# Optimization experiments

Measured on AMD Instinct MI355X. Metric: run time of the kernel, lower is better.

## Reference

```python
import jax, jax.numpy as jnp
import numpy as np

B, M, D, S, TOPK = 8, 4096, 512, 128, 64


def setup_inputs() -> dict:
    key = jax.random.key(0)
    ks = jax.random.split(key, 9)
    return {
        "memory": jax.random.normal(ks[0], (B, M, D), jnp.float32),
        "usage": jax.random.uniform(ks[1], (B, M), dtype=jnp.float32),
        "content": jax.random.normal(ks[2], (B, D), jnp.float32),
        "write_strength": jax.random.uniform(ks[3], (B, 1), dtype=jnp.float32),
        "query": jax.random.normal(ks[4], (B, S, D), jnp.float32),
        "key_proj_w": jax.random.normal(ks[5], (D, D), jnp.float32) * 0.02,
        "temporal_table": jax.random.normal(ks[6], (M, D), jnp.float32) * 0.02,
        "usage_decay": jnp.float32(0.99),
        "valid_mask": jax.random.randint(ks[7], (B, M), 0, 2) > 0,
        "write_index": jax.random.randint(ks[8], (B,), 0, M),
        "top_k": TOPK,
    }


def reference(memory, usage, content, write_strength, query, key_proj_w,
              temporal_table, usage_decay, valid_mask, write_index, top_k):
    # ---- write(): soft scatter into the slot selected by write_index ----
    idx = write_index % M                               # [B]
    temporal_emb = temporal_table[idx]                  # [B, D] gather
    content_wt = content + temporal_emb                 # [B, D]
    write_pos = jax.nn.one_hot(idx, M, dtype=memory.dtype)      # [B, M]
    a = write_pos[:, :, None] * write_strength[:, :, None]      # [B, M, 1]
    memory = memory * (1.0 - a) + content_wt[:, None, :] * a    # [B, M, D]
    valid = jnp.logical_or(valid_mask, write_pos > 0)           # [B, M]
    usage = usage * usage_decay + write_pos * write_strength    # [B, M]
    # ---- read(): content-based addressing with top-k masked softmax ----
    keys = jnp.einsum("bmd,ed->bme", memory, key_proj_w)        # Linear, no bias
    scores = jnp.einsum("bsd,bmd->bsm", query, keys) / (D ** 0.5)
    scores = jnp.where(valid[:, None, :], scores, -jnp.inf)
    top_vals = jax.lax.top_k(scores, top_k)[0]                  # [B, S, top_k]
    threshold = top_vals[..., -1:]                              # kth value
    scores = jnp.where(scores < threshold, -jnp.inf, scores)
    attn = jax.nn.softmax(scores, axis=-1)                      # [B, S, M]
    all_invalid = jnp.all(~valid, axis=-1)[:, None, None]
    attn = jnp.where(all_invalid, 0.0, attn)
    retrieved = jnp.einsum("bsm,bmd->bsd", attn, memory)        # [B, S, D]
    return retrieved, attn, usage
```

## Files before the change

kernel.cpp:

```cpp
#include <hip/hip_runtime.h>
#include <hip/hip_bf16.h>
#include <math.h>

#define BB 8
#define MM 4096
#define DD 512
#define SS 128

typedef short s16x8 __attribute__((ext_vector_type(8)));
typedef float f32x4 __attribute__((ext_vector_type(4)));

__device__ __forceinline__ unsigned short f2bf(float x) {
  unsigned u = __float_as_uint(x);
  unsigned r = u + 0x7fffu + ((u >> 16) & 1u);
  return (unsigned short)(r >> 16);
}
__device__ __forceinline__ float bf2f(unsigned short h) {
  return __uint_as_float(((unsigned)h) << 16);
}
__device__ __forceinline__ void split3(float x, unsigned short& s1,
                                       unsigned short& s2, unsigned short& s3) {
  s1 = f2bf(x);
  float r1 = x - bf2f(s1);
  s2 = f2bf(r1);
  float r2 = r1 - bf2f(s2);
  s3 = f2bf(r2);
}

__global__ __launch_bounds__(256) void update_kernel(
    float* __restrict__ memory, const float* __restrict__ usage,
    const float* __restrict__ content, const float* __restrict__ wstr,
    const float* __restrict__ ttab, const float* __restrict__ decay_p,
    const int* __restrict__ widx, float* __restrict__ usage_out) {
  const int b = blockIdx.x;
  int idx = widx[b] % MM; if (idx < 0) idx += MM;
  const float ws = wstr[b];
  const float decay = decay_p[0];
  for (int d = threadIdx.x; d < DD; d += blockDim.x) {
    float cw = content[b * DD + d] + ttab[(size_t)idx * DD + d];
    size_t off = (size_t)b * MM * DD + (size_t)idx * DD + d;
    float old = memory[off];
    memory[off] = old * (1.0f - ws) + cw * ws;
  }
  for (int m = threadIdx.x; m < MM; m += blockDim.x) {
    float u = usage[b * MM + m] * decay;
    if (m == idx) u += ws;
    usage_out[b * MM + m] = u;
  }
}

#define BMq 64
#define BNq 64
#define BKq 32
#define PADq 4

__global__ __launch_bounds__(256) void gemm_nn_qp(
    const float* __restrict__ A, const float* __restrict__ Bw,
    unsigned short* __restrict__ q1, unsigned short* __restrict__ q2,
    unsigned short* __restrict__ q3) {
  __shared__ __align__(16) float As[BKq][BMq + PADq];
  __shared__ __align__(16) float Bs[BKq][BNq + PADq];
  const int tid = threadIdx.x;
  const int tx = tid & 15, ty = tid >> 4;
  const int i0 = blockIdx.y * BMq;
  const int j0 = blockIdx.x * BNq;
  float acc[4][4] = {{0.f}};
  for (int k0 = 0; k0 < DD; k0 += BKq) {
#pragma unroll
    for (int r = 0; r < 2; ++r) {
      int ff = tid + r * 256;
      int row = ff >> 3, kq = ff & 7;
      float4 v = *(const float4*)(A + (size_t)(i0 + row) * DD + k0 + kq * 4);
      As[kq * 4 + 0][row] = v.x; As[kq * 4 + 1][row] = v.y;
      As[kq * 4 + 2][row] = v.z; As[kq * 4 + 3][row] = v.w;
      int kr = ff >> 4, jq = ff & 15;
      float4 w = *(const float4*)(Bw + (size_t)(k0 + kr) * DD + j0 + jq * 4);
      *(float4*)&Bs[kr][jq * 4] = w;
    }
    __syncthreads();
#pragma unroll
    for (int k = 0; k < BKq; ++k) {
      float4 a = *(const float4*)&As[k][ty * 4];
      float4 bb = *(const float4*)&Bs[k][tx * 4];
      float av[4] = {a.x, a.y, a.z, a.w};
      float bv[4] = {bb.x, bb.y, bb.z, bb.w};
#pragma unroll
      for (int i = 0; i < 4; ++i)
#pragma unroll
        for (int j = 0; j < 4; ++j) acc[i][j] += av[i] * bv[j];
    }
    __syncthreads();
  }
#pragma unroll
  for (int i = 0; i < 4; ++i) {
    int row = i0 + ty * 4 + i;
    ushort4 v1, v2, v3;
    split3(acc[i][0], v1.x, v2.x, v3.x);
    split3(acc[i][1], v1.y, v2.y, v3.y);
    split3(acc[i][2], v1.z, v2.z, v3.z);
    split3(acc[i][3], v1.w, v2.w, v3.w);
    *(ushort4*)(q1 + (size_t)row * DD + j0 + tx * 4) = v1;
    *(ushort4*)(q2 + (size_t)row * DD + j0 + tx * 4) = v2;
    *(ushort4*)(q3 + (size_t)row * DD + j0 + tx * 4) = v3;
  }
}

#define LSTR 40

__global__ __launch_bounds__(256, 2) void gemm_scores_mfma(
    const unsigned short* __restrict__ q1_g,
    const unsigned short* __restrict__ q2_g,
    const unsigned short* __restrict__ q3_g,
    const float* __restrict__ mem, float* __restrict__ sc_out) {
  __shared__ __align__(16) unsigned short q1_s[128 * LSTR];
  __shared__ __align__(16) unsigned short q2_s[128 * LSTR];
  __shared__ __align__(16) unsigned short q3_s[128 * LSTR];
  __shared__ __align__(16) unsigned short m1_s[64 * LSTR];
  __shared__ __align__(16) unsigned short m2_s[64 * LSTR];
  __shared__ __align__(16) unsigned short m3_s[64 * LSTR];
  const int tid = threadIdx.x;
  const int b = blockIdx.x & 7;
  const int j0 = (blockIdx.x >> 3) * 64;
  const int wv = tid >> 6, lane = tid & 63;
  const int quad = lane >> 4, r = lane & 15;

  const int qrow0 = tid >> 2, qc0 = tid & 3;
  const int qrow1 = (tid + 256) >> 2, qc1 = tid & 3;
  const unsigned short* q1b = q1_g + (size_t)b * SS * DD;
  const unsigned short* q2b = q2_g + (size_t)b * SS * DD;
  const unsigned short* q3b = q3_g + (size_t)b * SS * DD;
  const int mrow0 = tid >> 3, mk0 = tid & 7;
  const int mrow1 = (tid + 256) >> 3, mk1 = tid & 7;
  const float* mbase = mem + ((size_t)b * MM + j0) * DD;

  f32x4 accA[2][4], accB[2][4];
#pragma unroll
  for (int i = 0; i < 2; ++i)
#pragma unroll
    for (int j = 0; j < 4; ++j)
#pragma unroll
      for (int c = 0; c < 4; ++c) { accA[i][j][c] = 0.f; accB[i][j][c] = 0.f; }

  uint4 q1_r0, q1_r1, q2_r0, q2_r1, q3_r0, q3_r1;
  float4 m_r0, m_r1;

  q1_r0 = *(const uint4*)(q1b + (size_t)qrow0 * DD + qc0 * 8);
  q1_r1 = *(const uint4*)(q1b + (size_t)qrow1 * DD + qc1 * 8);
  q2_r0 = *(const uint4*)(q2b + (size_t)qrow0 * DD + qc0 * 8);
  q2_r1 = *(const uint4*)(q2b + (size_t)qrow1 * DD + qc1 * 8);
  q3_r0 = *(const uint4*)(q3b + (size_t)qrow0 * DD + qc0 * 8);
  q3_r1 = *(const uint4*)(q3b + (size_t)qrow1 * DD + qc1 * 8);
  m_r0 = *(const float4*)(mbase + (size_t)mrow0 * DD + mk0 * 4);
  m_r1 = *(const float4*)(mbase + (size_t)mrow1 * DD + mk1 * 4);

  for (int ks = 0; ks < 16; ++ks) {
    if (ks) __syncthreads();
    *(uint4*)&q1_s[qrow0 * LSTR + qc0 * 8] = q1_r0;
    *(uint4*)&q1_s[qrow1 * LSTR + qc1 * 8] = q1_r1;
    *(uint4*)&q2_s[qrow0 * LSTR + qc0 * 8] = q2_r0;
    *(uint4*)&q2_s[qrow1 * LSTR + qc1 * 8] = q2_r1;
    *(uint4*)&q3_s[qrow0 * LSTR + qc0 * 8] = q3_r0;
    *(uint4*)&q3_s[qrow1 * LSTR + qc1 * 8] = q3_r1;
    {
      ushort4 v1, v2, v3;
      split3(m_r0.x, v1.x, v2.x, v3.x);
      split3(m_r0.y, v1.y, v2.y, v3.y);
      split3(m_r0.z, v1.z, v2.z, v3.z);
      split3(m_r0.w, v1.w, v2.w, v3.w);
      *(ushort4*)&m1_s[mrow0 * LSTR + mk0 * 4] = v1;
      *(ushort4*)&m2_s[mrow0 * LSTR + mk0 * 4] = v2;
      *(ushort4*)&m3_s[mrow0 * LSTR + mk0 * 4] = v3;
      split3(m_r1.x, v1.x, v2.x, v3.x);
      split3(m_r1.y, v1.y, v2.y, v3.y);
      split3(m_r1.z, v1.z, v2.z, v3.z);
      split3(m_r1.w, v1.w, v2.w, v3.w);
      *(ushort4*)&m1_s[mrow1 * LSTR + mk1 * 4] = v1;
      *(ushort4*)&m2_s[mrow1 * LSTR + mk1 * 4] = v2;
      *(ushort4*)&m3_s[mrow1 * LSTR + mk1 * 4] = v3;
    }
    __syncthreads();
    if (ks < 15) {
      int k0 = (ks + 1) * 32;
      q1_r0 = *(const uint4*)(q1b + (size_t)qrow0 * DD + k0 + qc0 * 8);
      q1_r1 = *(const uint4*)(q1b + (size_t)qrow1 * DD + k0 + qc1 * 8);
      q2_r0 = *(const uint4*)(q2b + (size_t)qrow0 * DD + k0 + qc0 * 8);
      q2_r1 = *(const uint4*)(q2b + (size_t)qrow1 * DD + k0 + qc1 * 8);
      q3_r0 = *(const uint4*)(q3b + (size_t)qrow0 * DD + k0 + qc0 * 8);
      q3_r1 = *(const uint4*)(q3b + (size_t)qrow1 * DD + k0 + qc1 * 8);
      m_r0 = *(const float4*)(mbase + (size_t)mrow0 * DD + k0 + mk0 * 4);
      m_r1 = *(const float4*)(mbase + (size_t)mrow1 * DD + k0 + mk1 * 4);
    }
    s16x8 a1[2], a2[2], a3[2];
#pragma unroll
    for (int st = 0; st < 2; ++st) {
      int arow = wv * 32 + st * 16 + r;
      a1[st] = *(const s16x8*)&q1_s[arow * LSTR + quad * 8];
      a2[st] = *(const s16x8*)&q2_s[arow * LSTR + quad * 8];
      a3[st] = *(const s16x8*)&q3_s[arow * LSTR + quad * 8];
    }
#pragma unroll
    for (int jt = 0; jt < 4; ++jt) {
      int brow = jt * 16 + r;
      s16x8 b1 = *(const s16x8*)&m1_s[brow * LSTR + quad * 8];
      s16x8 b2 = *(const s16x8*)&m2_s[brow * LSTR + quad * 8];
      s16x8 b3 = *(const s16x8*)&m3_s[brow * LSTR + quad * 8];
#pragma unroll
      for (int st = 0; st < 2; ++st) {
        accB[st][jt] = __builtin_amdgcn_mfma_f32_16x16x32_bf16(a1[st], b3, accB[st][jt], 0, 0, 0);
        accB[st][jt] = __builtin_amdgcn_mfma_f32_16x16x32_bf16(a3[st], b1, accB[st][jt], 0, 0, 0);
        accB[st][jt] = __builtin_amdgcn_mfma_f32_16x16x32_bf16(a2[st], b2, accB[st][jt], 0, 0, 0);
        accB[st][jt] = __builtin_amdgcn_mfma_f32_16x16x32_bf16(a1[st], b2, accB[st][jt], 0, 0, 0);
        accB[st][jt] = __builtin_amdgcn_mfma_f32_16x16x32_bf16(a2[st], b1, accB[st][jt], 0, 0, 0);
        accA[st][jt] = __builtin_amdgcn_mfma_f32_16x16x32_bf16(a1[st], b1, accA[st][jt], 0, 0, 0);
      }
    }
  }
  const float scl = 0.04419417382415922f;
  float* C = sc_out + (size_t)b * SS * MM;
#pragma unroll
  for (int st = 0; st < 2; ++st)
#pragma unroll
    for (int jt = 0; jt < 4; ++jt)
#pragma unroll
      for (int reg = 0; reg < 4; ++reg) {
        int srow = wv * 32 + st * 16 + quad * 4 + reg;
        int scol = j0 + jt * 16 + r;
        C[(size_t)srow * MM + scol] = (accA[st][jt][reg] + accB[st][jt][reg]) * scl;
      }
}

__device__ __forceinline__ unsigned fkey(float f) {
  unsigned u = __float_as_uint(f);
  return (u & 0x80000000u) ? ~u : (u | 0x80000000u);
}
__device__ __forceinline__ float finv(unsigned u) {
  unsigned b = (u & 0x80000000u) ? (u & 0x7fffffffu) : ~u;
  return __uint_as_float(b);
}

__global__ __launch_bounds__(256) void select_kernel(
    const float* __restrict__ scores, const int* __restrict__ vmask,
    const int* __restrict__ widx, const int* __restrict__ topk,
    const float* __restrict__ memory, float* __restrict__ retrieved,
    float* __restrict__ attn) {
  __shared__ float sc[MM];
  __shared__ int kept[MM];
  __shared__ unsigned histw[4 * 256];
  __shared__ float red[256];
  __shared__ unsigned sh_pref;
  __shared__ int sh_k, sh_nkept;
  __shared__ float sh_zinv;

  const int tid = threadIdx.x;
  const int s = blockIdx.x, b = blockIdx.y;
  int wi = widx[b] % MM; if (wi < 0) wi += MM;
  const float4* srow4 = (const float4*)(scores + ((size_t)b * SS + s) * MM);
  const int4* vrow4 = (const int4*)(vmask + (size_t)b * MM);
  unsigned* hw = histw + (tid >> 6) * 256;

  if (tid == 0) { sh_pref = 0u; sh_nkept = 0; sh_k = topk[0]; }
  for (int i = tid; i < 1024; i += 256) histw[i] = 0u;
  __syncthreads();

  float lmax = -INFINITY;
  for (int m4 = tid; m4 < MM / 4; m4 += 256) {
    float4 v = srow4[m4];
    int4 mk = vrow4[m4];
    int mb = m4 * 4;
    if (!(mk.x || mb + 0 == wi)) v.x = -INFINITY;
    if (!(mk.y || mb + 1 == wi)) v.y = -INFINITY;
    if (!(mk.z || mb + 2 == wi)) v.z = -INFINITY;
    if (!(mk.w || mb + 3 == wi)) v.w = -INFINITY;
    ((float4*)sc)[m4] = v;
    lmax = fmaxf(lmax, fmaxf(fmaxf(v.x, v.y), fmaxf(v.z, v.w)));
    atomicAdd(&hw[fkey(v.x) >> 24], 1u);
    atomicAdd(&hw[fkey(v.y) >> 24], 1u);
    atomicAdd(&hw[fkey(v.z) >> 24], 1u);
    atomicAdd(&hw[fkey(v.w) >> 24], 1u);
  }
  red[tid] = lmax;
  __syncthreads();
#pragma unroll
  for (int off = 128; off > 0; off >>= 1) {
    if (tid < off) red[tid] = fmaxf(red[tid], red[tid + off]);
    __syncthreads();
  }
  const float maxv = red[0];

  for (int pass = 0; pass < 4; ++pass) {
    const int shift = 24 - pass * 8;
    if (pass > 0) {
      const unsigned pref = sh_pref;
      const unsigned hmask = 0xFFFFFFFFu << (shift + 8);
      for (int i = tid; i < 1024; i += 256) histw[i] = 0u;
      __syncthreads();
      for (int m = tid; m < MM; m += 256) {
        unsigned u = fkey(sc[m]);
        if ((u & hmask) == pref) atomicAdd(&hw[(u >> shift) & 0xFFu], 1u);
      }
      __syncthreads();
    }
    if (tid < 64) {
      const int l = tid;
      unsigned h0 = histw[l * 4 + 0] + histw[256 + l * 4 + 0] + histw[512 + l * 4 + 0] + histw[768 + l * 4 + 0];
      unsigned h1 = histw[l * 4 + 1] + histw[256 + l * 4 + 1] + histw[512 + l * 4 + 1] + histw[768 + l * 4 + 1];
      unsigned h2 = histw[l * 4 + 2] + histw[256 + l * 4 + 2] + histw[512 + l * 4 + 2] + histw[768 + l * 4 + 2];
      unsigned h3 = histw[l * 4 + 3] + histw[256 + l * 4 + 3] + histw[512 + l * 4 + 3] + histw[768 + l * 4 + 3];
      unsigned lsum = h0 + h1 + h2 + h3;
      unsigned g = lsum;
#pragma unroll
      for (int off = 1; off < 64; off <<= 1) {
        unsigned t = __shfl_down(g, off, 64);
        if (l + off < 64) g += t;
      }
      unsigned above = g - lsum;
      unsigned suf3 = h3 + above;
      unsigned suf2 = h2 + suf3;
      unsigned suf1 = h1 + suf2;
      unsigned suf0 = h0 + suf1;
      const unsigned kk = (unsigned)sh_k;
      const unsigned prefc = sh_pref;
      unsigned ge, geN;
      ge = suf0; geN = suf1;
      if (ge >= kk && geN < kk) { sh_pref = prefc | ((unsigned)(4 * l + 0) << shift); sh_k = (int)(kk - geN); }
      ge = suf1; geN = suf2;
      if (ge >= kk && geN < kk) { sh_pref = prefc | ((unsigned)(4 * l + 1) << shift); sh_k = (int)(kk - geN); }
      ge = suf2; geN = suf3;
      if (ge >= kk && geN < kk) { sh_pref = prefc | ((unsigned)(4 * l + 2) << shift); sh_k = (int)(kk - geN); }
      ge = suf3; geN = above;
      if (ge >= kk && geN < kk) { sh_pref = prefc | ((unsigned)(4 * l + 3) << shift); sh_k = (int)(kk - geN); }
    }
    __syncthreads();
  }
  const float thr = finv(sh_pref);

  float lz = 0.f;
  for (int m4 = tid; m4 < MM / 4; m4 += 256) {
    float4 v = ((float4*)sc)[m4];
    v.x = (v.x >= thr) ? __expf(v.x - maxv) : 0.f;
    v.y = (v.y >= thr) ? __expf(v.y - maxv) : 0.f;
    v.z = (v.z >= thr) ? __expf(v.z - maxv) : 0.f;
    v.w = (v.w >= thr) ? __expf(v.w - maxv) : 0.f;
    ((float4*)sc)[m4] = v;
    lz += v.x + v.y + v.z + v.w;
  }
  red[tid] = lz;
  __syncthreads();
#pragma unroll
  for (int off = 128; off > 0; off >>= 1) {
    if (tid < off) red[tid] += red[tid + off];
    __syncthreads();
  }
  if (tid == 0) sh_zinv = 1.0f / red[0];
  __syncthreads();
  const float zinv = sh_zinv;

  float4* arow4 = (float4*)(attn + ((size_t)b * SS + s) * MM);
  for (int m4 = tid; m4 < MM / 4; m4 += 256) {
    float4 p = ((float4*)sc)[m4];
    float4 o = make_float4(p.x * zinv, p.y * zinv, p.z * zinv, p.w * zinv);
    arow4[m4] = o;
    int mb = m4 * 4;
    if (p.x > 0.f) kept[atomicAdd(&sh_nkept, 1)] = mb + 0;
    if (p.y > 0.f) kept[atomicAdd(&sh_nkept, 1)] = mb + 1;
    if (p.z > 0.f) kept[atomicAdd(&sh_nkept, 1)] = mb + 2;
    if (p.w > 0.f) kept[atomicAdd(&sh_nkept, 1)] = mb + 3;
  }
  __syncthreads();
  const int nk = sh_nkept;

  float a0 = 0.f, a1 = 0.f;
  const float* mb_ = memory + (size_t)b * MM * DD;
  int i = 0;
  for (; i + 4 <= nk; i += 4) {
    int m0 = kept[i], m1 = kept[i + 1], m2 = kept[i + 2], m3 = kept[i + 3];
    float p0 = sc[m0], p1 = sc[m1], p2 = sc[m2], p3 = sc[m3];
    const float* r0 = mb_ + (size_t)m0 * DD;
    const float* r1 = mb_ + (size_t)m1 * DD;
    const float* r2 = mb_ + (size_t)m2 * DD;
    const float* r3 = mb_ + (size_t)m3 * DD;
    float v0a = r0[tid], v0b = r0[tid + 256];
    float v1a = r1[tid], v1b = r1[tid + 256];
    float v2a = r2[tid], v2b = r2[tid + 256];
    float v3a = r3[tid], v3b = r3[tid + 256];
    a0 += p0 * v0a + p1 * v1a + p2 * v2a + p3 * v3a;
    a1 += p0 * v0b + p1 * v1b + p2 * v2b + p3 * v3b;
  }
  for (; i < nk; ++i) {
    int m = kept[i];
    float p = sc[m];
    const float* mr = mb_ + (size_t)m * DD;
    a0 += p * mr[tid];
    a1 += p * mr[tid + 256];
  }
  float* rrow = retrieved + ((size_t)b * SS + s) * DD;
  rrow[tid] = a0 * zinv;
  rrow[tid + 256] = a1 * zinv;
}

extern "C" void kernel_launch(void* const* d_in, const int* in_sizes, int n_in,
                              void* d_out, int out_size, void* d_ws,
                              size_t ws_size, hipStream_t stream) {
  float* memory = (float*)d_in[0];
  const float* usage = (const float*)d_in[1];
  const float* content = (const float*)d_in[2];
  const float* wstr = (const float*)d_in[3];
  const float* query = (const float*)d_in[4];
  const float* W = (const float*)d_in[5];
  const float* ttab = (const float*)d_in[6];
  const float* decay = (const float*)d_in[7];
  const int* vmask = (const int*)d_in[8];
  const int* widx = (const int*)d_in[9];
  const int* topk = (const int*)d_in[10];

  float* out = (float*)d_out;
  float* retrieved = out;
  float* attn = out + (size_t)BB * SS * DD;
  float* usage_out = attn + (size_t)BB * SS * MM;

  const size_t qsz = (size_t)BB * SS * DD;
  float* scores = (float*)d_ws;
  unsigned short* q1 = (unsigned short*)(scores + (size_t)BB * SS * MM);
  unsigned short* q2 = q1 + qsz;
  unsigned short* q3;
  size_t need3 = (size_t)BB * SS * MM * 4 + 3 * qsz * 2;
  if (ws_size >= need3) {
    q3 = q2 + qsz;
  } else {
    q3 = (unsigned short*)(attn + (size_t)BB * SS * MM) - qsz;
  }

  update_kernel<<<BB, 256, 0, stream>>>(memory, usage, content, wstr, ttab,
                                        decay, widx, usage_out);
  gemm_nn_qp<<<dim3(DD / BNq, (BB * SS) / BMq), 256, 0, stream>>>(query, W, q1,
                                                                  q2, q3);
  gemm_scores_mfma<<<dim3((MM / 64) * BB), 256, 0, stream>>>(q1, q2, q3,
                                                             memory, scores);
  select_kernel<<<dim3(SS, BB), 256, 0, stream>>>(scores, vmask, widx, topk,
                                                  memory, retrieved, attn);
}
```

Before: 205.1 us.

## Widen scores GEMM tile to 128 memory rows per block and merge accumulators

Each block of the split-bf16 scores GEMM now covers 128 memory rows instead of 64, so each staged query tile in shared memory is reused across twice as many columns, and the grid is halved. The two separate accumulators (main term and correction terms) are merged into one, freeing registers for the larger tile. Occupancy drops to one block per CU via the launch bound, which may weaken latency hiding of the global loads and split conversion.

```diff
diff --git a/kernel.cpp b/kernel.cpp
--- a/kernel.cpp
+++ b/kernel.cpp
@@ -107,7 +107,7 @@
 
 #define LSTR 40
 
-__global__ __launch_bounds__(256, 2) void gemm_scores_mfma(
+__global__ __launch_bounds__(256, 1) void gemm_scores_mfma(
     const unsigned short* __restrict__ q1_g,
     const unsigned short* __restrict__ q2_g,
     const unsigned short* __restrict__ q3_g,
@@ -115,80 +115,76 @@
   __shared__ __align__(16) unsigned short q1_s[128 * LSTR];
   __shared__ __align__(16) unsigned short q2_s[128 * LSTR];
   __shared__ __align__(16) unsigned short q3_s[128 * LSTR];
-  __shared__ __align__(16) unsigned short m1_s[64 * LSTR];
-  __shared__ __align__(16) unsigned short m2_s[64 * LSTR];
-  __shared__ __align__(16) unsigned short m3_s[64 * LSTR];
+  __shared__ __align__(16) unsigned short m1_s[128 * LSTR];
+  __shared__ __align__(16) unsigned short m2_s[128 * LSTR];
+  __shared__ __align__(16) unsigned short m3_s[128 * LSTR];
   const int tid = threadIdx.x;
   const int b = blockIdx.x & 7;
-  const int j0 = (blockIdx.x >> 3) * 64;
+  const int j0 = (blockIdx.x >> 3) * 128;
   const int wv = tid >> 6, lane = tid & 63;
   const int quad = lane >> 4, r = lane & 15;
 
-  const int qrow0 = tid >> 2, qc0 = tid & 3;
-  const int qrow1 = (tid + 256) >> 2, qc1 = tid & 3;
+  const int qrow0 = tid >> 2, qc = tid & 3;
+  const int qrow1 = 64 + (tid >> 2);
   const unsigned short* q1b = q1_g + (size_t)b * SS * DD;
   const unsigned short* q2b = q2_g + (size_t)b * SS * DD;
   const unsigned short* q3b = q3_g + (size_t)b * SS * DD;
-  const int mrow0 = tid >> 3, mk0 = tid & 7;
-  const int mrow1 = (tid + 256) >> 3, mk1 = tid & 7;
+  const int mrow = tid >> 3, mk = tid & 7;
   const float* mbase = mem + ((size_t)b * MM + j0) * DD;
 
-  f32x4 accA[2][4], accB[2][4];
+  f32x4 acc[2][8];
 #pragma unroll
   for (int i = 0; i < 2; ++i)
 #pragma unroll
-    for (int j = 0; j < 4; ++j)
-#pragma unroll
-      for (int c = 0; c < 4; ++c) { accA[i][j][c] = 0.f; accB[i][j][c] = 0.f; }
-
-  uint4 q1_r0, q1_r1, q2_r0, q2_r1, q3_r0, q3_r1;
-  float4 m_r0, m_r1;
-
-  q1_r0 = *(const uint4*)(q1b + (size_t)qrow0 * DD + qc0 * 8);
-  q1_r1 = *(const uint4*)(q1b + (size_t)qrow1 * DD + qc1 * 8);
-  q2_r0 = *(const uint4*)(q2b + (size_t)qrow0 * DD + qc0 * 8);
-  q2_r1 = *(const uint4*)(q2b + (size_t)qrow1 * DD + qc1 * 8);
-  q3_r0 = *(const uint4*)(q3b + (size_t)qrow0 * DD + qc0 * 8);
-  q3_r1 = *(const uint4*)(q3b + (size_t)qrow1 * DD + qc1 * 8);
-  m_r0 = *(const float4*)(mbase + (size_t)mrow0 * DD + mk0 * 4);
-  m_r1 = *(const float4*)(mbase + (size_t)mrow1 * DD + mk1 * 4);
+    for (int j = 0; j < 8; ++j)
+#pragma unroll
+      for (int c = 0; c < 4; ++c) acc[i][j][c] = 0.f;
+
+  uint4 q1r0, q1r1, q2r0, q2r1, q3r0, q3r1;
+  float4 mr[4];
+
+  q1r0 = *(const uint4*)(q1b + (size_t)qrow0 * DD + qc * 8);
+  q1r1 = *(const uint4*)(q1b + (size_t)qrow1 * DD + qc * 8);
+  q2r0 = *(const uint4*)(q2b + (size_t)qrow0 * DD + qc * 8);
+  q2r1 = *(const uint4*)(q2b + (size_t)qrow1 * DD + qc * 8);
+  q3r0 = *(const uint4*)(q3b + (size_t)qrow0 * DD + qc * 8);
+  q3r1 = *(const uint4*)(q3b + (size_t)qrow1 * DD + qc * 8);
+#pragma unroll
+  for (int i = 0; i < 4; ++i)
+    mr[i] = *(const float4*)(mbase + (size_t)(mrow + 32 * i) * DD + mk * 4);
 
   for (int ks = 0; ks < 16; ++ks) {
     if (ks) __syncthreads();
-    *(uint4*)&q1_s[qrow0 * LSTR + qc0 * 8] = q1_r0;
-    *(uint4*)&q1_s[qrow1 * LSTR + qc1 * 8] = q1_r1;
-    *(uint4*)&q2_s[qrow0 * LSTR + qc0 * 8] = q2_r0;
-    *(uint4*)&q2_s[qrow1 * LSTR + qc1 * 8] = q2_r1;
-    *(uint4*)&q3_s[qrow0 * LSTR + qc0 * 8] = q3_r0;
-    *(uint4*)&q3_s[qrow1 * LSTR + qc1 * 8] = q3_r1;
-    {
+    *(uint4*)&q1_s[qrow0 * LSTR + qc * 8] = q1r0;
+    *(uint4*)&q1_s[qrow1 * LSTR + qc * 8] = q1r1;
+    *(uint4*)&q2_s[qrow0 * LSTR + qc * 8] = q2r0;
+    *(uint4*)&q2_s[qrow1 * LSTR + qc * 8] = q2r1;
+    *(uint4*)&q3_s[qrow0 * LSTR + qc * 8] = q3r0;
+    *(uint4*)&q3_s[qrow1 * LSTR + qc * 8] = q3r1;
+#pragma unroll
+    for (int i = 0; i < 4; ++i) {
       ushort4 v1, v2, v3;
-      split3(m_r0.x, v1.x, v2.x, v3.x);
-      split3(m_r0.y, v1.y, v2.y, v3.y);
-      split3(m_r0.z, v1.z, v2.z, v3.z);
-      split3(m_r0.w, v1.w, v2.w, v3.w);
-      *(ushort4*)&m1_s[mrow0 * LSTR + mk0 * 4] = v1;
-      *(ushort4*)&m2_s[mrow0 * LSTR + mk0 * 4] = v2;
-      *(ushort4*)&m3_s[mrow0 * LSTR + mk0 * 4] = v3;
-      split3(m_r1.x, v1.x, v2.x, v3.x);
-      split3(m_r1.y, v1.y, v2.y, v3.y);
-      split3(m_r1.z, v1.z, v2.z, v3.z);
-      split3(m_r1.w, v1.w, v2.w, v3.w);
-      *(ushort4*)&m1_s[mrow1 * LSTR + mk1 * 4] = v1;
-      *(ushort4*)&m2_s[mrow1 * LSTR + mk1 * 4] = v2;
-      *(ushort4*)&m3_s[mrow1 * LSTR + mk1 * 4] = v3;
+      split3(mr[i].x, v1.x, v2.x, v3.x);
+      split3(mr[i].y, v1.y, v2.y, v3.y);
+      split3(mr[i].z, v1.z, v2.z, v3.z);
+      split3(mr[i].w, v1.w, v2.w, v3.w);
+      int row = mrow + 32 * i;
+      *(ushort4*)&m1_s[row * LSTR + mk * 4] = v1;
+      *(ushort4*)&m2_s[row * LSTR + mk * 4] = v2;
+      *(ushort4*)&m3_s[row * LSTR + mk * 4] = v3;
     }
     __syncthreads();
     if (ks < 15) {
       int k0 = (ks + 1) * 32;
-      q1_r0 = *(const uint4*)(q1b + (size_t)qrow0 * DD + k0 + qc0 * 8);
-      q1_r1 = *(const uint4*)(q1b + (size_t)qrow1 * DD + k0 + qc1 * 8);
-      q2_r0 = *(const uint4*)(q2b + (size_t)qrow0 * DD + k0 + qc0 * 8);
-      q2_r1 = *(const uint4*)(q2b + (size_t)qrow1 * DD + k0 + qc1 * 8);
-      q3_r0 = *(const uint4*)(q3b + (size_t)qrow0 * DD + k0 + qc0 * 8);
-      q3_r1 = *(const uint4*)(q3b + (size_t)qrow1 * DD + k0 + qc1 * 8);
-      m_r0 = *(const float4*)(mbase + (size_t)mrow0 * DD + k0 + mk0 * 4);
-      m_r1 = *(const float4*)(mbase + (size_t)mrow1 * DD + k0 + mk1 * 4);
+      q1r0 = *(const uint4*)(q1b + (size_t)qrow0 * DD + k0 + qc * 8);
+      q1r1 = *(const uint4*)(q1b + (size_t)qrow1 * DD + k0 + qc * 8);
+      q2r0 = *(const uint4*)(q2b + (size_t)qrow0 * DD + k0 + qc * 8);
+      q2r1 = *(const uint4*)(q2b + (size_t)qrow1 * DD + k0 + qc * 8);
+      q3r0 = *(const uint4*)(q3b + (size_t)qrow0 * DD + k0 + qc * 8);
+      q3r1 = *(const uint4*)(q3b + (size_t)qrow1 * DD + k0 + qc * 8);
+#pragma unroll
+      for (int i = 0; i < 4; ++i)
+        mr[i] = *(const float4*)(mbase + (size_t)(mrow + 32 * i) * DD + k0 + mk * 4);
     }
     s16x8 a1[2], a2[2], a3[2];
 #pragma unroll
@@ -199,19 +195,19 @@
       a3[st] = *(const s16x8*)&q3_s[arow * LSTR + quad * 8];
     }
 #pragma unroll
-    for (int jt = 0; jt < 4; ++jt) {
+    for (int jt = 0; jt < 8; ++jt) {
       int brow = jt * 16 + r;
       s16x8 b1 = *(const s16x8*)&m1_s[brow * LSTR + quad * 8];
       s16x8 b2 = *(const s16x8*)&m2_s[brow * LSTR + quad * 8];
       s16x8 b3 = *(const s16x8*)&m3_s[brow * LSTR + quad * 8];
 #pragma unroll
       for (int st = 0; st < 2; ++st) {
-        accB[st][jt] = __builtin_amdgcn_mfma_f32_16x16x32_bf16(a1[st], b3, accB[st][jt], 0, 0, 0);
-        accB[st][jt] = __builtin_amdgcn_mfma_f32_16x16x32_bf16(a3[st], b1, accB[st][jt], 0, 0, 0);
-        accB[st][jt] = __builtin_amdgcn_mfma_f32_16x16x32_bf16(a2[st], b2, accB[st][jt], 0, 0, 0);
-        accB[st][jt] = __builtin_amdgcn_mfma_f32_16x16x32_bf16(a1[st], b2, accB[st][jt], 0, 0, 0);
-        accB[st][jt] = __builtin_amdgcn_mfma_f32_16x16x32_bf16(a2[st], b1, accB[st][jt], 0, 0, 0);
-        accA[st][jt] = __builtin_amdgcn_mfma_f32_16x16x32_bf16(a1[st], b1, accA[st][jt], 0, 0, 0);
+        acc[st][jt] = __builtin_amdgcn_mfma_f32_16x16x32_bf16(a1[st], b3, acc[st][jt], 0, 0, 0);
+        acc[st][jt] = __builtin_amdgcn_mfma_f32_16x16x32_bf16(a3[st], b1, acc[st][jt], 0, 0, 0);
+        acc[st][jt] = __builtin_amdgcn_mfma_f32_16x16x32_bf16(a2[st], b2, acc[st][jt], 0, 0, 0);
+        acc[st][jt] = __builtin_amdgcn_mfma_f32_16x16x32_bf16(a1[st], b2, acc[st][jt], 0, 0, 0);
+        acc[st][jt] = __builtin_amdgcn_mfma_f32_16x16x32_bf16(a2[st], b1, acc[st][jt], 0, 0, 0);
+        acc[st][jt] = __builtin_amdgcn_mfma_f32_16x16x32_bf16(a1[st], b1, acc[st][jt], 0, 0, 0);
       }
     }
   }
@@ -220,12 +216,12 @@
 #pragma unroll
   for (int st = 0; st < 2; ++st)
 #pragma unroll
-    for (int jt = 0; jt < 4; ++jt)
+    for (int jt = 0; jt < 8; ++jt)
 #pragma unroll
       for (int reg = 0; reg < 4; ++reg) {
         int srow = wv * 32 + st * 16 + quad * 4 + reg;
         int scol = j0 + jt * 16 + r;
-        C[(size_t)srow * MM + scol] = (accA[st][jt][reg] + accB[st][jt][reg]) * scl;
+        C[(size_t)srow * MM + scol] = acc[st][jt][reg] * scl;
       }
 }
 
@@ -434,8 +430,8 @@
                                         decay, widx, usage_out);
   gemm_nn_qp<<<dim3(DD / BNq, (BB * SS) / BMq), 256, 0, stream>>>(query, W, q1,
                                                                   q2, q3);
-  gemm_scores_mfma<<<dim3((MM / 64) * BB), 256, 0, stream>>>(q1, q2, q3,
-                                                             memory, scores);
+  gemm_scores_mfma<<<dim3((MM / 128) * BB), 256, 0, stream>>>(q1, q2, q3,
+                                                              memory, scores);
   select_kernel<<<dim3(SS, BB), 256, 0, stream>>>(scores, vmask, widx, topk,
                                                   memory, retrieved, attn);
 }
```

Result: no change. 203.4 us (-0.8%).
